# Kernel optimization log

Measured on AMD Instinct MI355X. Metric: run time of the kernel, lower is better.

## Reference

```python
import jax, jax.numpy as jnp
import numpy as np

# Standard JPEG luminance quantization table (quality 50)
_QTABLE = np.array([
    [16, 11, 10, 16, 24, 40, 51, 61],
    [12, 12, 14, 19, 26, 58, 60, 55],
    [14, 13, 16, 24, 40, 57, 69, 56],
    [14, 17, 22, 29, 51, 87, 80, 62],
    [18, 22, 37, 56, 68, 109, 103, 77],
    [24, 35, 55, 64, 81, 104, 113, 92],
    [49, 64, 78, 87, 103, 121, 120, 101],
    [72, 92, 95, 98, 112, 100, 103, 99]], dtype=np.float32)

def _dct_mtx(n=8):
    # Orthonormal DCT-II basis matrix: mtx @ block @ mtx.T is the 2-D DCT,
    # so mtx.T @ coeffs @ mtx is the inverse DCT used by this module.
    k = np.arange(n)[:, None]
    j = np.arange(n)[None, :]
    m = np.cos(np.pi * (2 * j + 1) * k / (2 * n)) * np.sqrt(2.0 / n)
    m[0, :] /= np.sqrt(2.0)
    return m.astype(np.float32)

def setup_inputs() -> dict:
    key = jax.random.key(0)
    B, C, H, W = 32, 1, 1024, 1024  # square image required by the reshape chain
    x = jax.random.normal(key, (B, C, H, W), dtype=jnp.float32) * 10.0
    return {
        "x": x,
        "qtable": jnp.asarray(_QTABLE),
        "mtx": jnp.asarray(_dct_mtx(8)),
    }

def reference(x, qtable, mtx):
    B, D1, D2, D3 = x.shape
    # view -> permute -> reshape chain extracting 8x8 blocks (faithful to torch code)
    y = x.reshape(B, D1 * D2 // 8, 8, D3)
    y = jnp.transpose(y, (0, 1, 3, 2))                       # (B, D1*D2/8, D3, 8)
    y = y.reshape(B, D1 * D2 * D3 // 64, 8, 8)
    y = jnp.transpose(y, (0, 1, 3, 2))                       # (B, Nblk, 8, 8)
    y = y * qtable                                           # dequantize
    # mtx.T @ y @ mtx  (batched tiny 8x8 IDCT)
    y = jnp.einsum('ji,bnjk,kl->bnil', mtx, y, mtx)
    # inverse reshape/permute chain back to image layout
    y = jnp.transpose(y, (0, 1, 3, 2))
    y = y.reshape(B, D1 * D2 // 8, D2, 8)
    y = jnp.transpose(y, (0, 1, 3, 2))
    return y.reshape(x.shape) + 128.0
```

## Files before the change

kernel.cpp:

```cpp
#include <hip/hip_runtime.h>


__global__ __launch_bounds__(256, 8) void bidct_kernel(
    const float* __restrict__ x, const float* __restrict__ qt,
    const float* __restrict__ mtx, float* __restrict__ out)
{
    __shared__ float tile[2048];
    __shared__ float sM[64];
    __shared__ float sQ[64];

    const int t = threadIdx.x;
    if (t < 64) { sM[t] = mtx[t]; sQ[t] = qt[t]; }
    __syncthreads();

    const int w = blockIdx.x;
    const int base = (w >> 2) * 8192 + (w & 3) * 256;

    float4* tile4 = reinterpret_cast<float4*>(tile);
    const float4* sM4 = reinterpret_cast<const float4*>(sM);

#pragma unroll
    for (int r = 0; r < 2; ++r) {
        const int f  = r * 256 + t;
        const int j  = f >> 6;
        const int c4 = f & 63;
        float4 v = *reinterpret_cast<const float4*>(x + base + j * 1024 + c4 * 4);
        const int k0 = (c4 & 1) * 4;
        v.x *= sQ[j * 8 + k0 + 0];
        v.y *= sQ[j * 8 + k0 + 1];
        v.z *= sQ[j * 8 + k0 + 2];
        v.w *= sQ[j * 8 + k0 + 3];
        tile4[f] = v;
    }
    __syncthreads();

    const int bl = t >> 3;
    const int i  = t & 7;

    float T[8] = {0.f, 0.f, 0.f, 0.f, 0.f, 0.f, 0.f, 0.f};
#pragma unroll
    for (int j = 0; j < 8; ++j) {
        const float m = sM[j * 8 + i];
        const float4 xa = tile4[j * 64 + bl * 2];
        const float4 xb = tile4[j * 64 + bl * 2 + 1];
        T[0] = fmaf(m, xa.x, T[0]);
        T[1] = fmaf(m, xa.y, T[1]);
        T[2] = fmaf(m, xa.z, T[2]);
        T[3] = fmaf(m, xa.w, T[3]);
        T[4] = fmaf(m, xb.x, T[4]);
        T[5] = fmaf(m, xb.y, T[5]);
        T[6] = fmaf(m, xb.z, T[6]);
        T[7] = fmaf(m, xb.w, T[7]);
    }

    float o[8] = {128.f, 128.f, 128.f, 128.f, 128.f, 128.f, 128.f, 128.f};
#pragma unroll
    for (int k = 0; k < 8; ++k) {
        const float4 m0 = sM4[k * 2];
        const float4 m1 = sM4[k * 2 + 1];
        o[0] = fmaf(T[k], m0.x, o[0]);
        o[1] = fmaf(T[k], m0.y, o[1]);
        o[2] = fmaf(T[k], m0.z, o[2]);
        o[3] = fmaf(T[k], m0.w, o[3]);
        o[4] = fmaf(T[k], m1.x, o[4]);
        o[5] = fmaf(T[k], m1.y, o[5]);
        o[6] = fmaf(T[k], m1.z, o[6]);
        o[7] = fmaf(T[k], m1.w, o[7]);
    }
    __syncthreads();

    tile4[i * 64 + bl * 2]     = make_float4(o[0], o[1], o[2], o[3]);
    tile4[i * 64 + bl * 2 + 1] = make_float4(o[4], o[5], o[6], o[7]);
    __syncthreads();

#pragma unroll
    for (int r = 0; r < 2; ++r) {
        const int f  = r * 256 + t;
        const int j  = f >> 6;
        const int c4 = f & 63;
        *reinterpret_cast<float4*>(out + base + j * 1024 + c4 * 4) = tile4[f];
    }
}

extern "C" void kernel_launch(void* const* d_in, const int* in_sizes, int n_in,
                              void* d_out, int out_size, void* d_ws, size_t ws_size,
                              hipStream_t stream) {
    const float* x   = (const float*)d_in[0];
    const float* qt  = (const float*)d_in[1];
    const float* mtx = (const float*)d_in[2];
    float*       out = (float*)d_out;

    const int grid = out_size / 2048;
    bidct_kernel<<<grid, 256, 0, stream>>>(x, qt, mtx, out);
}
```

Baseline: 231.3 us.

## Assign one full 8x8 block per thread, dropping shared-memory tiling

Each thread now loads a whole 8x8 block directly from global memory, dequantizes it, performs both IDCT matrix products in registers, and writes the block back. The shared-memory staging, barriers and cooperative coalesced loads go away, and the DCT and quantization tables are read through scalar global loads. In exchange each thread issues strided 32-byte row accesses across 8 rows. It also holds 64 accumulators in registers, which may raise register pressure and lower occupancy.

```diff
diff --git a/kernel.cpp b/kernel.cpp
--- a/kernel.cpp
+++ b/kernel.cpp
@@ -1,84 +1,71 @@
 #include <hip/hip_runtime.h>
 
 
-__global__ __launch_bounds__(256, 8) void bidct_kernel(
+__global__ __launch_bounds__(256) void bidct_kernel(
     const float* __restrict__ x, const float* __restrict__ qt,
     const float* __restrict__ mtx, float* __restrict__ out)
 {
-    __shared__ float tile[2048];
-    __shared__ float sM[64];
-    __shared__ float sQ[64];
+    const int n   = blockIdx.x * 256 + threadIdx.x;
+    const int img = n >> 14;
+    const int m   = n & 16383;
+    const int br  = m >> 7;
+    const int bc  = m & 127;
+    const size_t base = ((size_t)img << 20) + ((size_t)br << 13) + ((size_t)bc << 3);
 
-    const int t = threadIdx.x;
-    if (t < 64) { sM[t] = mtx[t]; sQ[t] = qt[t]; }
-    __syncthreads();
+    const float* __restrict__ px = x + base;
 
-    const int w = blockIdx.x;
-    const int base = (w >> 2) * 8192 + (w & 3) * 256;
-
-    float4* tile4 = reinterpret_cast<float4*>(tile);
-    const float4* sM4 = reinterpret_cast<const float4*>(sM);
+    float T[8][8];
+#pragma unroll
+    for (int i = 0; i < 8; ++i)
+#pragma unroll
+        for (int k = 0; k < 8; ++k)
+            T[i][k] = 0.0f;
 
 #pragma unroll
-    for (int r = 0; r < 2; ++r) {
-        const int f  = r * 256 + t;
-        const int j  = f >> 6;
-        const int c4 = f & 63;
-        float4 v = *reinterpret_cast<const float4*>(x + base + j * 1024 + c4 * 4);
-        const int k0 = (c4 & 1) * 4;
-        v.x *= sQ[j * 8 + k0 + 0];
-        v.y *= sQ[j * 8 + k0 + 1];
-        v.z *= sQ[j * 8 + k0 + 2];
-        v.w *= sQ[j * 8 + k0 + 3];
-        tile4[f] = v;
-    }
-    __syncthreads();
-
-    const int bl = t >> 3;
-    const int i  = t & 7;
-
-    float T[8] = {0.f, 0.f, 0.f, 0.f, 0.f, 0.f, 0.f, 0.f};
+    for (int jh = 0; jh < 2; ++jh) {
+        float4 xa[4], xb[4];
 #pragma unroll
-    for (int j = 0; j < 8; ++j) {
-        const float m = sM[j * 8 + i];
-        const float4 xa = tile4[j * 64 + bl * 2];
-        const float4 xb = tile4[j * 64 + bl * 2 + 1];
-        T[0] = fmaf(m, xa.x, T[0]);
-        T[1] = fmaf(m, xa.y, T[1]);
-        T[2] = fmaf(m, xa.z, T[2]);
-        T[3] = fmaf(m, xa.w, T[3]);
-        T[4] = fmaf(m, xb.x, T[4]);
-        T[5] = fmaf(m, xb.y, T[5]);
-        T[6] = fmaf(m, xb.z, T[6]);
-        T[7] = fmaf(m, xb.w, T[7]);
+        for (int jj = 0; jj < 4; ++jj) {
+            const float* row = px + (size_t)(jh * 4 + jj) * 1024;
+            xa[jj] = *reinterpret_cast<const float4*>(row);
+            xb[jj] = *reinterpret_cast<const float4*>(row + 4);
+        }
+#pragma unroll
+        for (int jj = 0; jj < 4; ++jj) {
+            const int j = jh * 4 + jj;
+            float xq[8];
+            xq[0] = xa[jj].x * qt[j * 8 + 0];
+            xq[1] = xa[jj].y * qt[j * 8 + 1];
+            xq[2] = xa[jj].z * qt[j * 8 + 2];
+            xq[3] = xa[jj].w * qt[j * 8 + 3];
+            xq[4] = xb[jj].x * qt[j * 8 + 4];
+            xq[5] = xb[jj].y * qt[j * 8 + 5];
+            xq[6] = xb[jj].z * qt[j * 8 + 6];
+            xq[7] = xb[jj].w * qt[j * 8 + 7];
+#pragma unroll
+            for (int i = 0; i < 8; ++i) {
+                const float mji = mtx[j * 8 + i];
+#pragma unroll
+                for (int k = 0; k < 8; ++k)
+                    T[i][k] = fmaf(mji, xq[k], T[i][k]);
+            }
+        }
     }
 
-    float o[8] = {128.f, 128.f, 128.f, 128.f, 128.f, 128.f, 128.f, 128.f};
+    float* __restrict__ po = out + base;
 #pragma unroll
-    for (int k = 0; k < 8; ++k) {
-        const float4 m0 = sM4[k * 2];
-        const float4 m1 = sM4[k * 2 + 1];
-        o[0] = fmaf(T[k], m0.x, o[0]);
-        o[1] = fmaf(T[k], m0.y, o[1]);
-        o[2] = fmaf(T[k], m0.z, o[2]);
-        o[3] = fmaf(T[k], m0.w, o[3]);
-        o[4] = fmaf(T[k], m1.x, o[4]);
-        o[5] = fmaf(T[k], m1.y, o[5]);
-        o[6] = fmaf(T[k], m1.z, o[6]);
-        o[7] = fmaf(T[k], m1.w, o[7]);
-    }
-    __syncthreads();
-
-    tile4[i * 64 + bl * 2]     = make_float4(o[0], o[1], o[2], o[3]);
-    tile4[i * 64 + bl * 2 + 1] = make_float4(o[4], o[5], o[6], o[7]);
-    __syncthreads();
-
+    for (int i = 0; i < 8; ++i) {
+        float o[8] = {128.f, 128.f, 128.f, 128.f, 128.f, 128.f, 128.f, 128.f};
 #pragma unroll
-    for (int r = 0; r < 2; ++r) {
-        const int f  = r * 256 + t;
-        const int j  = f >> 6;
-        const int c4 = f & 63;
-        *reinterpret_cast<float4*>(out + base + j * 1024 + c4 * 4) = tile4[f];
+        for (int k = 0; k < 8; ++k) {
+            const float tk = T[i][k];
+#pragma unroll
+            for (int l = 0; l < 8; ++l)
+                o[l] = fmaf(tk, mtx[k * 8 + l], o[l]);
+        }
+        float* row = po + (size_t)i * 1024;
+        *reinterpret_cast<float4*>(row)     = make_float4(o[0], o[1], o[2], o[3]);
+        *reinterpret_cast<float4*>(row + 4) = make_float4(o[4], o[5], o[6], o[7]);
     }
 }
 
@@ -90,6 +77,7 @@
     const float* mtx = (const float*)d_in[2];
     float*       out = (float*)d_out;
 
-    const int grid = out_size / 2048;
+    const int total_blocks = out_size / 64;
+    const int grid         = total_blocks / 256;
     bidct_kernel<<<grid, 256, 0, stream>>>(x, qt, mtx, out);
 }
```

Result: no change. 233.0 us (+0.8%).
